# Performance work log

Measured on AMD Instinct MI355X. Metric: run time of the kernel, lower is better.

The kernel has to match this reference:

```python
import jax, jax.numpy as jnp
import numpy as np

N_NODES = 100000


def _gin_layer(x, edge_index, Wa, ba, Wb, bb):
    # GINConv, eps=0: h_i = MLP(x_i + sum_{j->i} x_j)
    src, dst = edge_index[0], edge_index[1]
    agg = jax.ops.segment_sum(x[src], dst, num_segments=N_NODES)  # [N, d]
    h = x + agg
    h = jax.nn.relu(h @ Wa + ba) @ Wb + bb
    return h


def setup_inputs() -> dict:
    key = jax.random.key(0)
    ks = jax.random.split(key, 8)
    d_in, d_h, E = 128, 128, 1600000
    scale_in = 1.0 / np.sqrt(d_in)
    scale_h = 1.0 / np.sqrt(d_h)
    return {
        "x": jax.random.normal(ks[0], (N_NODES, d_in), dtype=jnp.float32),
        "edge_index": jax.random.randint(ks[1], (2, E), 0, N_NODES, dtype=jnp.int64),
        "batch": jnp.zeros((N_NODES,), dtype=jnp.int64),
        "W1a": jax.random.normal(ks[2], (d_in, d_h), dtype=jnp.float32) * scale_in,
        "b1a": jnp.zeros((d_h,), dtype=jnp.float32),
        "W1b": jax.random.normal(ks[3], (d_h, d_h), dtype=jnp.float32) * scale_h,
        "b1b": jnp.zeros((d_h,), dtype=jnp.float32),
        "W2a": jax.random.normal(ks[4], (d_h, d_h), dtype=jnp.float32) * scale_h,
        "b2a": jnp.zeros((d_h,), dtype=jnp.float32),
        "W2b": jax.random.normal(ks[5], (d_h, d_h), dtype=jnp.float32) * scale_h,
        "b2b": jnp.zeros((d_h,), dtype=jnp.float32),
    }


def reference(x, edge_index, batch, W1a, b1a, W1b, b1b, W2a, b2a, W2b, b2b):
    h = jax.nn.relu(_gin_layer(x, edge_index, W1a, b1a, W1b, b1b))
    h = jax.nn.relu(_gin_layer(h, edge_index, W2a, b2a, W2b, b2b))
    return h
```

## Files before the change

kernel.cpp:

```cpp
#include <hip/hip_runtime.h>
#include <hip/hip_bf16.h>

#define D 128
#define EPB 4096
#define CAP 6144

typedef float f32x4 __attribute__((ext_vector_type(4)));
typedef float f32x2 __attribute__((ext_vector_type(2)));
typedef short short8 __attribute__((ext_vector_type(8)));


__device__ __forceinline__ unsigned bf16_rtn_bits(float x) {
    unsigned u = __float_as_uint(x);
    return (u + 0x7fffu + ((u >> 16) & 1u)) >> 16;
}

__device__ __forceinline__ f32x2 pkadd(f32x2 a, f32x2 b) {
    f32x2 d;
    asm("v_pk_add_f32 %0, %1, %2" : "=v"(d) : "v"(a), "v"(b));
    return d;
}

__device__ __forceinline__ void addbf8p(f32x2* acc, uint4 v) {
    f32x2 p0 = {__uint_as_float(v.x << 16), __uint_as_float(v.x & 0xffff0000u)};
    f32x2 p1 = {__uint_as_float(v.y << 16), __uint_as_float(v.y & 0xffff0000u)};
    f32x2 p2 = {__uint_as_float(v.z << 16), __uint_as_float(v.z & 0xffff0000u)};
    f32x2 p3 = {__uint_as_float(v.w << 16), __uint_as_float(v.w & 0xffff0000u)};
    acc[0] = pkadd(acc[0], p0);
    acc[1] = pkadd(acc[1], p1);
    acc[2] = pkadd(acc[2], p2);
    acc[3] = pkadd(acc[3], p3);
}


__global__ __launch_bounds__(256) void k_prep(const float* __restrict__ W1a, const float* __restrict__ W1b,
                                              const float* __restrict__ W2a, const float* __restrict__ W2b,
                                              unsigned short* __restrict__ Wt,
                                              const float4* __restrict__ X, uint4* __restrict__ O,
                                              int n8, int* __restrict__ gz, int nzero) {
    if (blockIdx.x < 256) {
        int m = blockIdx.x >> 6;
        int i = (blockIdx.x & 63) * 256 + threadIdx.x;
        const float* W = (m == 0) ? W1a : (m == 1) ? W1b : (m == 2) ? W2a : W2b;
        int k = i >> 7, n = i & 127;
        Wt[m * 16384 + n * 128 + k] = (unsigned short)bf16_rtn_bits(W[i]);
        return;
    }
    int i = (blockIdx.x - 256) * 256 + threadIdx.x;
    if (i < nzero) gz[i] = 0;
    if (i >= n8) return;
    float4 a = X[2 * i], b = X[2 * i + 1];
    uint4 o;
    o.x = bf16_rtn_bits(a.x) | (bf16_rtn_bits(a.y) << 16);
    o.y = bf16_rtn_bits(a.z) | (bf16_rtn_bits(a.w) << 16);
    o.z = bf16_rtn_bits(b.x) | (bf16_rtn_bits(b.y) << 16);
    o.w = bf16_rtn_bits(b.z) | (bf16_rtn_bits(b.w) << 16);
    O[i] = o;
}


__global__ __launch_bounds__(256) void k_bin(const int* __restrict__ src,
                                             const int* __restrict__ dst, int E,
                                             int* __restrict__ gCursor,
                                             unsigned* __restrict__ binned) {
    __shared__ int cnt[512];
    __shared__ int offs[512];
    __shared__ int c2[512];
    __shared__ int gOff[512];
    __shared__ int s[256];
    __shared__ unsigned staged[EPB];
    __shared__ unsigned short bo[EPB];
    int t = threadIdx.x;
    cnt[t] = 0; cnt[t + 256] = 0;
    c2[t] = 0; c2[t + 256] = 0;
    __syncthreads();

    unsigned pk[EPB / 256];
    int bk[EPB / 256];
    int e0 = blockIdx.x * EPB;
#pragma unroll
    for (int i = 0; i < EPB / 256; ++i) {
        int e = e0 + i * 256 + t;
        int b = -1; unsigned p = 0;
        if (e < E) {
            int dv = dst[e], sv = src[e];
            b = dv >> 8;
            p = ((unsigned)sv << 8) | (unsigned)(dv & 255);
            atomicAdd(&cnt[b], 1);
        }
        pk[i] = p; bk[i] = b;
    }
    __syncthreads();
    int v0 = cnt[2 * t], v1 = cnt[2 * t + 1];
    int ps = v0 + v1;
    s[t] = ps;
    __syncthreads();
    for (int off = 1; off < 256; off <<= 1) {
        int tv = (t >= off) ? s[t - off] : 0;
        __syncthreads();
        s[t] += tv;
        __syncthreads();
    }
    int ex = s[t] - ps;
    offs[2 * t] = ex;
    offs[2 * t + 1] = ex + v0;
    if (cnt[2 * t])     gOff[2 * t]     = atomicAdd(&gCursor[2 * t], cnt[2 * t]);
    if (cnt[2 * t + 1]) gOff[2 * t + 1] = atomicAdd(&gCursor[2 * t + 1], cnt[2 * t + 1]);
    __syncthreads();
#pragma unroll
    for (int i = 0; i < EPB / 256; ++i) {
        int b = bk[i];
        if (b >= 0) {
            int p = offs[b] + atomicAdd(&c2[b], 1);
            staged[p] = pk[i];
            bo[p] = (unsigned short)b;
        }
    }
    __syncthreads();
    int total = s[255];
    for (int p = t; p < total; p += 256) {
        int b = bo[p];
        binned[(size_t)b * CAP + gOff[b] + (p - offs[b])] = staged[p];
    }
}

__global__ __launch_bounds__(256) void k_csr(const unsigned* __restrict__ binned,
                                             const int* __restrict__ bucketCnt,
                                             int* __restrict__ alloc,
                                             int2* __restrict__ rowse,
                                             int* __restrict__ colA,
                                             int Nn) {
    __shared__ int hist[256], loc[256], cur[256], s[256];
    __shared__ int baseSh;
    int t = threadIdx.x, b = blockIdx.x;
    int n = bucketCnt[b];
    const unsigned* bp = binned + (size_t)b * CAP;
    hist[t] = 0; cur[t] = 0;
    __syncthreads();
    for (int i = t; i < n; i += 256) atomicAdd(&hist[bp[i] & 255u], 1);
    __syncthreads();
    int v = hist[t];
    s[t] = v;
    __syncthreads();
    for (int off = 1; off < 256; off <<= 1) {
        int tv = (t >= off) ? s[t - off] : 0;
        __syncthreads();
        s[t] += tv;
        __syncthreads();
    }
    loc[t] = s[t] - v;
    if (t == 255) baseSh = atomicAdd(alloc, s[255]);
    __syncthreads();
    int base = baseSh;
    int node = b * 256 + t;
    if (node < Nn) rowse[node] = make_int2(base + loc[t], base + loc[t] + v);
    for (int i = t; i < n; i += 256) {
        unsigned w = bp[i];
        int dl = (int)(w & 255u);
        int p = atomicAdd(&cur[dl], 1);
        colA[base + loc[dl] + p] = (int)(w >> 8);
    }
}


__global__ __launch_bounds__(256) void agg_bf16(const unsigned short* __restrict__ X,
                                                const int2* __restrict__ rowse,
                                                const int* __restrict__ colA,
                                                unsigned short* __restrict__ H, int nnodes) {
    int node = blockIdx.x * 4 + (threadIdx.x >> 6);
    if (node >= nnodes) return;
    int lane = threadIdx.x & 63;
    int qt = lane >> 4, slot = lane & 15;
    const uint4* x4 = (const uint4*)X;
    size_t base = (size_t)node * 16 + slot;

    int2 se = rowse[node];
    int e = se.x, end = se.y;

    f32x2 acc[4] = {{0.f, 0.f}, {0.f, 0.f}, {0.f, 0.f}, {0.f, 0.f}};
    f32x2 acc2[4] = {{0.f, 0.f}, {0.f, 0.f}, {0.f, 0.f}, {0.f, 0.f}};
    if (qt == 0) addbf8p(acc, x4[base]);

    for (; e + 16 <= end; e += 16) {
        int s0 = colA[e + qt];
        int s1 = colA[e + 4 + qt];
        int s2 = colA[e + 8 + qt];
        int s3 = colA[e + 12 + qt];
        uint4 v0 = x4[(size_t)s0 * 16 + slot];
        uint4 v1 = x4[(size_t)s1 * 16 + slot];
        uint4 v2 = x4[(size_t)s2 * 16 + slot];
        uint4 v3 = x4[(size_t)s3 * 16 + slot];
        addbf8p(acc, v0);
        addbf8p(acc2, v1);
        addbf8p(acc, v2);
        addbf8p(acc2, v3);
    }
    if (e + 8 <= end) {
        int s0 = colA[e + qt];
        int s1 = colA[e + 4 + qt];
        uint4 v0 = x4[(size_t)s0 * 16 + slot];
        uint4 v1 = x4[(size_t)s1 * 16 + slot];
        addbf8p(acc, v0);
        addbf8p(acc2, v1);
        e += 8;
    }
    for (; e < end; e += 4) {
        int idx = e + qt;
        if (idx < end) {
            int s = colA[idx];
            addbf8p(acc, x4[(size_t)s * 16 + slot]);
        }
    }
    float a8[8];
#pragma unroll
    for (int j = 0; j < 4; ++j) {
        f32x2 t = pkadd(acc[j], acc2[j]);
        a8[2 * j] = t[0];
        a8[2 * j + 1] = t[1];
    }
#pragma unroll
    for (int j = 0; j < 8; ++j) {
        a8[j] += __shfl_xor(a8[j], 16);
        a8[j] += __shfl_xor(a8[j], 32);
    }
    if (qt == 0) {
        uint4 o;
        o.x = bf16_rtn_bits(a8[0]) | (bf16_rtn_bits(a8[1]) << 16);
        o.y = bf16_rtn_bits(a8[2]) | (bf16_rtn_bits(a8[3]) << 16);
        o.z = bf16_rtn_bits(a8[4]) | (bf16_rtn_bits(a8[5]) << 16);
        o.w = bf16_rtn_bits(a8[6]) | (bf16_rtn_bits(a8[7]) << 16);
        ((uint4*)H)[base] = o;
    }
}


template <bool OUT_BF16>
__global__ __launch_bounds__(256) void mlp_mfma(const unsigned short* __restrict__ Hb,
                                                const unsigned short* __restrict__ WaT,
                                                const float* __restrict__ ba,
                                                const unsigned short* __restrict__ WbT,
                                                const float* __restrict__ bb,
                                                void* __restrict__ OutP, int nrows) {
    __shared__ unsigned short sh[2][64 * 128];
    const int tid = threadIdx.x;
    const int wv = tid >> 6, l = tid & 63, q = l >> 4, cl = l & 15;
    const int ntiles = (nrows + 63) >> 6;

    short8 B1[2][4], B2[2][4];
    float bva[2], bvb[2];
#pragma unroll
    for (int cf = 0; cf < 2; ++cf) {
        const unsigned short* wa = WaT + (size_t)(wv * 32 + cf * 16 + cl) * 128 + q * 8;
        const unsigned short* wb = WbT + (size_t)(wv * 32 + cf * 16 + cl) * 128 + q * 8;
#pragma unroll
        for (int kk = 0; kk < 4; ++kk) {
            B1[cf][kk] = *(const short8*)(wa + kk * 32);
            B2[cf][kk] = *(const short8*)(wb + kk * 32);
        }
        bva[cf] = ba[wv * 32 + cf * 16 + cl];
        bvb[cf] = bb[wv * 32 + cf * 16 + cl];
    }

    int tile = blockIdx.x;
    if (tile >= ntiles) return;

    {
        const int rows0 = tile * 64;
        const int nvalid = min(64, nrows - rows0);
        const uint4* src = (const uint4*)(Hb + (size_t)rows0 * 128);
#pragma unroll
        for (int it = 0; it < 4; ++it) {
            int idx = it * 256 + tid;
            int row = idx >> 4, s16 = idx & 15;
            uint4 v = {0u, 0u, 0u, 0u};
            if (row < nvalid) v = src[idx];
            int byteoff = (row << 8) + ((s16 << 4) ^ ((row & 7) << 4));
            *(uint4*)((char*)&sh[0][0] + byteoff) = v;
        }
    }
    int cur = 0;
    __syncthreads();

    while (true) {
        const int rows0 = tile * 64;
        const int nvalid = min(64, nrows - rows0);
        const int nexttile = tile + (int)gridDim.x;
        const bool havenext = nexttile < ntiles;

        uint4 r[4];
        if (havenext) {
            const int nr0 = nexttile * 64;
            const int nnv = min(64, nrows - nr0);
            const uint4* src = (const uint4*)(Hb + (size_t)nr0 * 128);
#pragma unroll
            for (int it = 0; it < 4; ++it) {
                int idx = it * 256 + tid;
                int row = idx >> 4;
                uint4 v = {0u, 0u, 0u, 0u};
                if (row < nnv) v = src[idx];
                r[it] = v;
            }
        }

        const char* shc = (const char*)&sh[cur][0];
        f32x4 acc[4][2];
#pragma unroll
        for (int cf = 0; cf < 2; ++cf) {
            f32x4 a = {bva[cf], bva[cf], bva[cf], bva[cf]};
#pragma unroll
            for (int m = 0; m < 4; ++m) acc[m][cf] = a;
        }
#pragma unroll
        for (int kk = 0; kk < 4; ++kk) {
            short8 a[4];
#pragma unroll
            for (int m = 0; m < 4; ++m) {
                int row = m * 16 + cl;
                int byteoff = (row << 8) + ((kk * 64 + q * 16) ^ ((row & 7) << 4));
                a[m] = *(const short8*)(shc + byteoff);
            }
#pragma unroll
            for (int m = 0; m < 4; ++m)
#pragma unroll
                for (int cf = 0; cf < 2; ++cf)
                    acc[m][cf] = __builtin_amdgcn_mfma_f32_16x16x32_bf16(a[m], B1[cf][kk], acc[m][cf], 0, 0, 0);
        }
        __syncthreads();

#pragma unroll
        for (int m = 0; m < 4; ++m)
#pragma unroll
            for (int cf = 0; cf < 2; ++cf)
#pragma unroll
                for (int rr = 0; rr < 4; ++rr) {
                    int row = m * 16 + q * 4 + rr;
                    int col = wv * 32 + cf * 16 + cl;
                    int byteoff = (row << 8) + ((col * 2) ^ ((row & 7) << 4));
                    *(unsigned short*)((char*)&sh[cur][0] + byteoff) =
                        (unsigned short)bf16_rtn_bits(fmaxf(acc[m][cf][rr], 0.f));
                }
        __syncthreads();

#pragma unroll
        for (int cf = 0; cf < 2; ++cf) {
            f32x4 a = {bvb[cf], bvb[cf], bvb[cf], bvb[cf]};
#pragma unroll
            for (int m = 0; m < 4; ++m) acc[m][cf] = a;
        }
#pragma unroll
        for (int kk = 0; kk < 4; ++kk) {
            short8 a[4];
#pragma unroll
            for (int m = 0; m < 4; ++m) {
                int row = m * 16 + cl;
                int byteoff = (row << 8) + ((kk * 64 + q * 16) ^ ((row & 7) << 4));
                a[m] = *(const short8*)(shc + byteoff);
            }
#pragma unroll
            for (int m = 0; m < 4; ++m)
#pragma unroll
                for (int cf = 0; cf < 2; ++cf)
                    acc[m][cf] = __builtin_amdgcn_mfma_f32_16x16x32_bf16(a[m], B2[cf][kk], acc[m][cf], 0, 0, 0);
        }

#pragma unroll
        for (int m = 0; m < 4; ++m)
#pragma unroll
            for (int cf = 0; cf < 2; ++cf)
#pragma unroll
                for (int rr = 0; rr < 4; ++rr) {
                    int row = m * 16 + q * 4 + rr;
                    if (row < nvalid) {
                        float v = fmaxf(acc[m][cf][rr], 0.f);
                        size_t gi = ((size_t)rows0 + row) * 128 + wv * 32 + cf * 16 + cl;
                        if (OUT_BF16)
                            ((unsigned short*)OutP)[gi] = (unsigned short)bf16_rtn_bits(v);
                        else
                            ((float*)OutP)[gi] = v;
                    }
                }

        if (!havenext) break;
#pragma unroll
        for (int it = 0; it < 4; ++it) {
            int idx = it * 256 + tid;
            int row = idx >> 4, s16 = idx & 15;
            int byteoff = (row << 8) + ((s16 << 4) ^ ((row & 7) << 4));
            *(uint4*)((char*)&sh[cur ^ 1][0] + byteoff) = r[it];
        }
        __syncthreads();
        cur ^= 1;
        tile = nexttile;
    }
}


extern "C" void kernel_launch(void* const* d_in, const int* in_sizes, int n_in,
                              void* d_out, int out_size, void* d_ws, size_t ws_size,
                              hipStream_t stream) {
    const float* x  = (const float*)d_in[0];
    const int*   ei = (const int*)d_in[1];
    const float* W1a = (const float*)d_in[3];
    const float* b1a = (const float*)d_in[4];
    const float* W1b = (const float*)d_in[5];
    const float* b1b = (const float*)d_in[6];
    const float* W2a = (const float*)d_in[7];
    const float* b2a = (const float*)d_in[8];
    const float* W2b = (const float*)d_in[9];
    const float* b2b = (const float*)d_in[10];
    float* out = (float*)d_out;

    const int Nn = in_sizes[0] / D;
    const int E  = in_sizes[1] / 2;
    const int* srcIdx = ei;
    const int* dstIdx = ei + E;
    const int NB = (Nn + 255) >> 8;

    char* w = (char*)d_ws;
    size_t off = 0;
    int2* rowse = (int2*)(w + off);    off += (size_t)Nn * 8;
    off = (off + 255) & ~(size_t)255;
    int* gCursor = (int*)(w + off);    off += (size_t)(NB + 1) * 4;
    int* alloc = gCursor + NB;
    off = (off + 255) & ~(size_t)255;
    int* colA = (int*)(w + off);       off += (size_t)E * 4;
    off = (off + 255) & ~(size_t)255;
    unsigned short* wsp = (unsigned short*)(w + off); off += (size_t)4 * 16384 * 2;
    off = (off + 255) & ~(size_t)255;
    unsigned short* bufA = (unsigned short*)(w + off); off += (size_t)Nn * 128 * 2;
    off = (off + 255) & ~(size_t)255;
    unsigned short* bufB = (unsigned short*)(w + off);
    unsigned* binned = (unsigned*)bufB;

    unsigned short* W1aT = wsp + 0 * 16384;
    unsigned short* W1bT = wsp + 1 * 16384;
    unsigned short* W2aT = wsp + 2 * 16384;
    unsigned short* W2bT = wsp + 3 * 16384;

    const int gBin = (E + EPB - 1) / EPB;
    const int gPrep = 256 + (Nn * 16 + 255) / 256;

    k_prep<<<gPrep, 256, 0, stream>>>(W1a, W1b, W2a, W2b, wsp,
                                      (const float4*)x, (uint4*)bufA, Nn * 16, gCursor, NB + 1);

    k_bin<<<gBin, 256, 0, stream>>>(srcIdx, dstIdx, E, gCursor, binned);
    k_csr<<<NB, 256, 0, stream>>>(binned, gCursor, alloc, rowse, colA, Nn);

    const int gAgg = (Nn + 3) / 4;
    const int gMlp = 512;

    agg_bf16<<<gAgg, 256, 0, stream>>>(bufA, rowse, colA, bufB, Nn);
    mlp_mfma<true><<<gMlp, 256, 0, stream>>>(bufB, W1aT, b1a, W1bT, b1b, (void*)bufA, Nn);
    agg_bf16<<<gAgg, 256, 0, stream>>>(bufA, rowse, colA, bufB, Nn);
    mlp_mfma<false><<<gMlp, 256, 0, stream>>>(bufB, W2aT, b2a, W2bT, b2b, (void*)out, Nn);
}
```

Measured before the change: 218.1 us.

## Fuse CSR construction with first-layer aggregation using per-quarter shared column lists

The CSR build kernel is split into four blocks per 256-node bucket, each handling 64 destination nodes. Each block keeps its column indices in shared memory and performs the first GIN aggregation directly, writing into the output buffer as scratch. This removes one aggregation launch and the global re-read of colA/rowse for layer one. The MLP grid size is also changed to depend on the tile count. The fused kernel rescans each bucket four times and drops parallelism in the gather phase, with each wave handling 16 nodes serially.

```diff
diff --git a/kernel.cpp b/kernel.cpp
--- a/kernel.cpp
+++ b/kernel.cpp
@@ -4,6 +4,7 @@
 #define D 128
 #define EPB 4096
 #define CAP 6144
+#define CAPQ 2048
 
 typedef float f32x4 __attribute__((ext_vector_type(4)));
 typedef float f32x2 __attribute__((ext_vector_type(2)));
@@ -124,41 +125,123 @@
     }
 }
 
-__global__ __launch_bounds__(256) void k_csr(const unsigned* __restrict__ binned,
-                                             const int* __restrict__ bucketCnt,
-                                             int* __restrict__ alloc,
-                                             int2* __restrict__ rowse,
-                                             int* __restrict__ colA,
-                                             int Nn) {
-    __shared__ int hist[256], loc[256], cur[256], s[256];
+
+__global__ __launch_bounds__(256) void k_csragg(const unsigned* __restrict__ binned,
+                                                const int* __restrict__ bucketCnt,
+                                                int* __restrict__ alloc,
+                                                const unsigned short* __restrict__ Xb,
+                                                int2* __restrict__ rowse,
+                                                int* __restrict__ colA,
+                                                unsigned short* __restrict__ H,
+                                                int Nn) {
+    __shared__ int hist[64], loc[64], cur[64], s64[64];
+    __shared__ int colL[CAPQ];
     __shared__ int baseSh;
-    int t = threadIdx.x, b = blockIdx.x;
-    int n = bucketCnt[b];
+    const int t = threadIdx.x;
+    const int b = blockIdx.x >> 2;
+    const int qd = blockIdx.x & 3;
+    const int n = bucketCnt[b];
     const unsigned* bp = binned + (size_t)b * CAP;
-    hist[t] = 0; cur[t] = 0;
-    __syncthreads();
-    for (int i = t; i < n; i += 256) atomicAdd(&hist[bp[i] & 255u], 1);
-    __syncthreads();
-    int v = hist[t];
-    s[t] = v;
-    __syncthreads();
-    for (int off = 1; off < 256; off <<= 1) {
-        int tv = (t >= off) ? s[t - off] : 0;
-        __syncthreads();
-        s[t] += tv;
-        __syncthreads();
-    }
-    loc[t] = s[t] - v;
-    if (t == 255) baseSh = atomicAdd(alloc, s[255]);
-    __syncthreads();
-    int base = baseSh;
-    int node = b * 256 + t;
-    if (node < Nn) rowse[node] = make_int2(base + loc[t], base + loc[t] + v);
+
+    if (t < 64) { hist[t] = 0; cur[t] = 0; }
+    __syncthreads();
     for (int i = t; i < n; i += 256) {
         unsigned w = bp[i];
         int dl = (int)(w & 255u);
-        int p = atomicAdd(&cur[dl], 1);
-        colA[base + loc[dl] + p] = (int)(w >> 8);
+        if ((dl >> 6) == qd) atomicAdd(&hist[dl & 63], 1);
+    }
+    __syncthreads();
+    if (t < 64) s64[t] = hist[t];
+    __syncthreads();
+    for (int off = 1; off < 64; off <<= 1) {
+        int v = 0;
+        if (t < 64 && t >= off) v = s64[t - off];
+        __syncthreads();
+        if (t < 64) s64[t] += v;
+        __syncthreads();
+    }
+    if (t < 64) loc[t] = s64[t] - hist[t];
+    if (t == 63) baseSh = atomicAdd(alloc, s64[63]);
+    __syncthreads();
+    const int base = baseSh;
+    for (int i = t; i < n; i += 256) {
+        unsigned w = bp[i];
+        int dl = (int)(w & 255u);
+        if ((dl >> 6) == qd) {
+            int l = dl & 63;
+            int p = loc[l] + atomicAdd(&cur[l], 1);
+            int sI = (int)(w >> 8);
+            colL[p] = sI;
+            colA[base + p] = sI;
+        }
+    }
+    if (t < 64) {
+        int node = b * 256 + qd * 64 + t;
+        if (node < Nn) rowse[node] = make_int2(base + loc[t], base + loc[t] + hist[t]);
+    }
+    __syncthreads();
+
+    const int wv = t >> 6, lane = t & 63, qt = lane >> 4, slot = lane & 15;
+    const uint4* x4 = (const uint4*)Xb;
+    for (int i = 0; i < 16; ++i) {
+        int ln = wv * 16 + i;
+        int node = b * 256 + qd * 64 + ln;
+        if (node >= Nn) break;
+        size_t rbase = (size_t)node * 16 + slot;
+        f32x2 acc[4] = {{0.f, 0.f}, {0.f, 0.f}, {0.f, 0.f}, {0.f, 0.f}};
+        f32x2 acc2[4] = {{0.f, 0.f}, {0.f, 0.f}, {0.f, 0.f}, {0.f, 0.f}};
+        if (qt == 0) addbf8p(acc, x4[rbase]);
+        int e = loc[ln], end = loc[ln] + hist[ln];
+        for (; e + 16 <= end; e += 16) {
+            int s0 = colL[e + qt];
+            int s1 = colL[e + 4 + qt];
+            int s2 = colL[e + 8 + qt];
+            int s3 = colL[e + 12 + qt];
+            uint4 v0 = x4[(size_t)s0 * 16 + slot];
+            uint4 v1 = x4[(size_t)s1 * 16 + slot];
+            uint4 v2 = x4[(size_t)s2 * 16 + slot];
+            uint4 v3 = x4[(size_t)s3 * 16 + slot];
+            addbf8p(acc, v0);
+            addbf8p(acc2, v1);
+            addbf8p(acc, v2);
+            addbf8p(acc2, v3);
+        }
+        if (e + 8 <= end) {
+            int s0 = colL[e + qt];
+            int s1 = colL[e + 4 + qt];
+            uint4 v0 = x4[(size_t)s0 * 16 + slot];
+            uint4 v1 = x4[(size_t)s1 * 16 + slot];
+            addbf8p(acc, v0);
+            addbf8p(acc2, v1);
+            e += 8;
+        }
+        for (; e < end; e += 4) {
+            int idx = e + qt;
+            if (idx < end) {
+                int s = colL[idx];
+                addbf8p(acc, x4[(size_t)s * 16 + slot]);
+            }
+        }
+        float a8[8];
+#pragma unroll
+        for (int j = 0; j < 4; ++j) {
+            f32x2 tt = pkadd(acc[j], acc2[j]);
+            a8[2 * j] = tt[0];
+            a8[2 * j + 1] = tt[1];
+        }
+#pragma unroll
+        for (int j = 0; j < 8; ++j) {
+            a8[j] += __shfl_xor(a8[j], 16);
+            a8[j] += __shfl_xor(a8[j], 32);
+        }
+        if (qt == 0) {
+            uint4 o;
+            o.x = bf16_rtn_bits(a8[0]) | (bf16_rtn_bits(a8[1]) << 16);
+            o.y = bf16_rtn_bits(a8[2]) | (bf16_rtn_bits(a8[3]) << 16);
+            o.z = bf16_rtn_bits(a8[4]) | (bf16_rtn_bits(a8[5]) << 16);
+            o.w = bf16_rtn_bits(a8[6]) | (bf16_rtn_bits(a8[7]) << 16);
+            ((uint4*)H)[rbase] = o;
+        }
     }
 }
 
@@ -431,6 +514,7 @@
     off = (off + 255) & ~(size_t)255;
     unsigned short* bufB = (unsigned short*)(w + off);
     unsigned* binned = (unsigned*)bufB;
+    unsigned short* h1 = (unsigned short*)d_out;
 
     unsigned short* W1aT = wsp + 0 * 16384;
     unsigned short* W1bT = wsp + 1 * 16384;
@@ -439,18 +523,16 @@
 
     const int gBin = (E + EPB - 1) / EPB;
     const int gPrep = 256 + (Nn * 16 + 255) / 256;
+    const int ntiles = (Nn + 63) / 64;
+    const int gMlp = (ntiles + 2) / 3;
 
     k_prep<<<gPrep, 256, 0, stream>>>(W1a, W1b, W2a, W2b, wsp,
                                       (const float4*)x, (uint4*)bufA, Nn * 16, gCursor, NB + 1);
 
     k_bin<<<gBin, 256, 0, stream>>>(srcIdx, dstIdx, E, gCursor, binned);
-    k_csr<<<NB, 256, 0, stream>>>(binned, gCursor, alloc, rowse, colA, Nn);
-
-    const int gAgg = (Nn + 3) / 4;
-    const int gMlp = 512;
-
-    agg_bf16<<<gAgg, 256, 0, stream>>>(bufA, rowse, colA, bufB, Nn);
-    mlp_mfma<true><<<gMlp, 256, 0, stream>>>(bufB, W1aT, b1a, W1bT, b1b, (void*)bufA, Nn);
-    agg_bf16<<<gAgg, 256, 0, stream>>>(bufA, rowse, colA, bufB, Nn);
+
+    k_csragg<<<NB * 4, 256, 0, stream>>>(binned, gCursor, alloc, bufA, rowse, colA, h1, Nn);
+    mlp_mfma<true><<<gMlp, 256, 0, stream>>>(h1, W1aT, b1a, W1bT, b1b, (void*)bufA, Nn);
+    agg_bf16<<<(Nn + 3) / 4, 256, 0, stream>>>(bufA, rowse, colA, bufB, Nn);
     mlp_mfma<false><<<gMlp, 256, 0, stream>>>(bufB, W2aT, b2a, W2bT, b2b, (void*)out, Nn);
 }
```

Result: slower. 248.4 us (+13.9%).
